# Kernel tuning notes

Measured on AMD Instinct MI355X. Metric: run time of the kernel, lower is better.

The kernel has to match this reference:

```python
import jax, jax.numpy as jnp
import numpy as np

HDIM = 64

def setup_inputs() -> dict:
    key = jax.random.key(0)
    ks = jax.random.split(key, 5)
    B, T, D = 4, 2048, 1024
    x = jax.random.normal(ks[0], (B, T, D), dtype=jnp.float32)
    s = 1.0 / np.sqrt(D)
    W_qkv = jax.random.normal(ks[1], (D, 3 * D), dtype=jnp.float32) * s
    b_qkv = jax.random.normal(ks[2], (3 * D,), dtype=jnp.float32) * 0.02
    W_out = jax.random.normal(ks[3], (D, D), dtype=jnp.float32) * s
    b_out = jax.random.normal(ks[4], (D,), dtype=jnp.float32) * 0.02
    return {"x": x, "W_qkv": W_qkv, "b_qkv": b_qkv, "W_out": W_out, "b_out": b_out}

def reference(x, W_qkv, b_qkv, W_out, b_out):
    B, T, D = x.shape
    H = D // HDIM
    qkv = x @ W_qkv + b_qkv                          # [B,T,3D]
    q, k, v = jnp.split(qkv, 3, axis=-1)
    # [B,T,D] -> [B,H,T,Hdim]
    q = q.reshape(B, T, H, HDIM).transpose(0, 2, 1, 3)
    k = k.reshape(B, T, H, HDIM).transpose(0, 2, 1, 3)
    v = v.reshape(B, T, H, HDIM).transpose(0, 2, 1, 3)
    scores = jnp.einsum('bhqd,bhkd->bhqk', q, k) / jnp.sqrt(jnp.float32(HDIM))
    causal = jnp.tril(jnp.ones((T, T), dtype=bool))
    scores = jnp.where(causal[None, None], scores, -jnp.inf)
    weights = jax.nn.softmax(scores, axis=-1)        # dropout_prob=0 -> identity
    out = jnp.einsum('bhqk,bhkd->bhqd', weights, v)  # [B,H,T,Hdim]
    out = out.transpose(0, 2, 1, 3).reshape(B, T, D)
    return out @ W_out + b_out
```

## Files before the change

### kernel.cpp

```cpp
#include <hip/hip_runtime.h>

typedef __attribute__((ext_vector_type(8))) short short8;
typedef __attribute__((ext_vector_type(4))) short s16x4;
typedef __attribute__((ext_vector_type(4))) float f32x4;

#define AS1 __attribute__((address_space(1)))
#define AS3 __attribute__((address_space(3)))

__device__ __forceinline__ void gload_lds16(const void* g, void* l) {
  __builtin_amdgcn_global_load_lds((const AS1 void*)g, (AS3 void*)l, 16, 0, 0);
}

__device__ __forceinline__ unsigned short f2bf(float f) {
  unsigned int u = __float_as_uint(f);
  u += 0x7fffu + ((u >> 16) & 1u);
  return (unsigned short)(u >> 16);
}

__global__ __launch_bounds__(256) void k_convert(const float* __restrict__ in,
                                                 unsigned short* __restrict__ out) {
  long i = (long)blockIdx.x * 256 + threadIdx.x;
  const float4* p = (const float4*)in + i * 2;
  float4 a = p[0], b = p[1];
  short8 o;
  o[0] = (short)f2bf(a.x); o[1] = (short)f2bf(a.y);
  o[2] = (short)f2bf(a.z); o[3] = (short)f2bf(a.w);
  o[4] = (short)f2bf(b.x); o[5] = (short)f2bf(b.y);
  o[6] = (short)f2bf(b.z); o[7] = (short)f2bf(b.w);
  ((short8*)out)[i] = o;
}

__global__ __launch_bounds__(256) void k_transpose_w(const float* __restrict__ w,
                                                     unsigned short* __restrict__ wt,
                                                     int K, int N) {
  __shared__ float t[64][65];
  const int tilesN = N >> 6;
  const int tk = blockIdx.x / tilesN, tn = blockIdx.x % tilesN;
  const int c = threadIdx.x & 63, r0 = (threadIdx.x >> 6) * 16;
#pragma unroll
  for (int i = 0; i < 16; ++i)
    t[r0 + i][c] = w[(long)(tk * 64 + r0 + i) * N + tn * 64 + c];
  __syncthreads();
#pragma unroll
  for (int i = 0; i < 16; ++i)
    wt[(long)(tn * 64 + r0 + i) * K + tk * 64 + c] = f2bf(t[c][r0 + i]);
}

__global__ __launch_bounds__(256) void k_transpose_v(const unsigned short* __restrict__ qkv,
                                                     unsigned short* __restrict__ vt) {
  __shared__ __align__(16) unsigned short t[64][72];
  const int tt = blockIdx.x & 31, bh = blockIdx.x >> 5;
  const int b = bh >> 4, h = bh & 15;
  const int r = threadIdx.x >> 2, c0 = (threadIdx.x & 3) * 16;
  const unsigned short* src = qkv + (long)(b * 2048 + tt * 64 + r) * 3072 + 2048 + h * 64 + c0;
  *(short8*)&t[r][c0] = *(const short8*)src;
  *(short8*)&t[r][c0 + 8] = *(const short8*)(src + 8);
  __syncthreads();
  short8 w0, w1;
#pragma unroll
  for (int i = 0; i < 8; ++i) w0[i] = (short)t[c0 + i][r];
#pragma unroll
  for (int i = 0; i < 8; ++i) w1[i] = (short)t[c0 + 8 + i][r];
  unsigned short* dst = vt + (long)(bh * 64 + r) * 2048 + tt * 64 + c0;
  *(short8*)dst = w0;
  *(short8*)(dst + 8) = w1;
}

template <int OUT_BF16>
__global__ __launch_bounds__(256) void k_gemm(const unsigned short* __restrict__ A,
                                              const unsigned short* __restrict__ BT,
                                              const float* __restrict__ bias,
                                              void* __restrict__ out,
                                              int M, int N, int K) {
  __shared__ __align__(16) unsigned short As[128 * 64];
  __shared__ __align__(16) unsigned short Bs[128 * 64];
  const int tid = threadIdx.x, lane = tid & 63, wid = tid >> 6;
  const int r16 = lane & 15, khi = lane >> 4;
  const int wr = wid >> 1, wc = wid & 1;
  const int tilesN = N >> 7;
  const int tm = blockIdx.x / tilesN, tn = blockIdx.x % tilesN;
  const long m0 = (long)tm * 128, n0 = (long)tn * 128;
  f32x4 acc[4][4] = {};
  const int srow = tid >> 3, scol = (tid & 7) * 8;

  for (int k0 = 0; k0 < K; k0 += 64) {
#pragma unroll
    for (int call = 0; call < 4; ++call) {
      int row = call * 32 + srow;
      gload_lds16(A + (m0 + row) * K + k0 + scol, &As[call * 2048 + wid * 512]);
      gload_lds16(BT + (n0 + row) * K + k0 + scol, &Bs[call * 2048 + wid * 512]);
    }
    __syncthreads();
#pragma unroll
    for (int kk = 0; kk < 2; ++kk) {
      short8 af[4], bf[4];
#pragma unroll
      for (int m = 0; m < 4; ++m)
        af[m] = *(const short8*)&As[(wr * 64 + m * 16 + r16) * 64 + kk * 32 + khi * 8];
#pragma unroll
      for (int n = 0; n < 4; ++n)
        bf[n] = *(const short8*)&Bs[(wc * 64 + n * 16 + r16) * 64 + kk * 32 + khi * 8];
#pragma unroll
      for (int m = 0; m < 4; ++m)
#pragma unroll
        for (int n = 0; n < 4; ++n)
          acc[m][n] = __builtin_amdgcn_mfma_f32_16x16x32_bf16(af[m], bf[n], acc[m][n], 0, 0, 0);
    }
    __syncthreads();
  }
#pragma unroll
  for (int m = 0; m < 4; ++m) {
    long row = m0 + wr * 64 + m * 16 + khi * 4;
#pragma unroll
    for (int n = 0; n < 4; ++n) {
      int col = (int)n0 + wc * 64 + n * 16 + r16;
      float bv = bias[col];
#pragma unroll
      for (int j = 0; j < 4; ++j) {
        float v = acc[m][n][j] + bv;
        if (OUT_BF16)
          ((unsigned short*)out)[(row + j) * N + col] = f2bf(v);
        else
          ((float*)out)[(row + j) * N + col] = v;
      }
    }
  }
}

__global__ __launch_bounds__(512) void k_attn(const unsigned short* __restrict__ qkv,
                                              const unsigned short* __restrict__ vt,
                                              unsigned short* __restrict__ aout) {
  __shared__ __align__(16) unsigned short Ks[2][64 * 64];
  __shared__ __align__(16) unsigned short VTs[2][64 * 64];
  __shared__ __align__(16) unsigned short Ps[8][16 * 72];
  const int tid = threadIdx.x, lane = tid & 63, wid = tid >> 6;
  const int r16 = lane & 15, khi = lane >> 4;
  const int qt = 15 - (int)(blockIdx.x >> 6), bh = blockIdx.x & 63;
  const int b = bh >> 4, h = bh & 15;
  const long qrow0 = (long)b * 2048 + qt * 128;

  const int srow = wid * 8 + (lane >> 3);
  const int lck = (lane & 7) ^ (srow & 7);
  const unsigned short* kbase =
      qkv + ((long)b * 2048 + srow) * 3072 + 1024 + h * 64 + lck * 8;
  const unsigned short* vbase = vt + ((long)bh * 64 + srow) * 2048 + lck * 8;

  const long qrow = qrow0 + wid * 16 + r16;
  const short8 qf0 = *(const short8*)&qkv[qrow * 3072 + h * 64 + khi * 8];
  const short8 qf1 = *(const short8*)&qkv[qrow * 3072 + h * 64 + 32 + khi * 8];

  gload_lds16(kbase, &Ks[0][wid * 512]);
  gload_lds16(vbase, &VTs[0][wid * 512]);

  const int ktmax = 2 * qt + 1;
  const int ktw = (qt * 128 + wid * 16 + 15) >> 6;
  const int qg = qt * 128 + wid * 16 + r16;
  float m_run = -1e30f, l_run = 0.f;
  f32x4 o[4] = {};

  for (int kt = 0; kt <= ktmax; ++kt) {
    const int cur = kt & 1;
    __builtin_amdgcn_s_barrier();
    if (kt < ktmax) {
      gload_lds16(kbase + (long)(kt + 1) * 64 * 3072, &Ks[cur ^ 1][wid * 512]);
      gload_lds16(vbase + (kt + 1) * 64, &VTs[cur ^ 1][wid * 512]);
      asm volatile("s_waitcnt vmcnt(2)" ::: "memory");
    } else {
      asm volatile("s_waitcnt vmcnt(0)" ::: "memory");
    }
    __builtin_amdgcn_s_barrier();
    if (kt > ktw) continue;

    f32x4 s[4] = {};
    __builtin_amdgcn_s_setprio(1);
#pragma unroll
    for (int kk = 0; kk < 2; ++kk) {
      const int pc = ((kk * 4 + khi) ^ (r16 & 7)) * 8;
      const short8 qf = kk ? qf1 : qf0;
#pragma unroll
      for (int n = 0; n < 4; ++n) {
        short8 kf = *(const short8*)&Ks[cur][(n * 16 + r16) * 64 + pc];
        s[n] = __builtin_amdgcn_mfma_f32_16x16x32_bf16(kf, qf, s[n], 0, 0, 0);
      }
    }
    __builtin_amdgcn_s_setprio(0);

    const bool need_mask = (kt * 64 + 63) > (qt * 128 + wid * 16);
    const int ktB = kt * 64;
#pragma unroll
    for (int n = 0; n < 4; ++n)
#pragma unroll
      for (int j = 0; j < 4; ++j) {
        float v = s[n][j] * 0.125f;
        if (need_mask && (ktB + n * 16 + khi * 4 + j) > qg) v = -1e30f;
        s[n][j] = v;
      }

    float pm = s[0][0];
#pragma unroll
    for (int n = 0; n < 4; ++n)
#pragma unroll
      for (int j = 0; j < 4; ++j) pm = fmaxf(pm, s[n][j]);
    pm = fmaxf(pm, __shfl_xor(pm, 16, 64));
    pm = fmaxf(pm, __shfl_xor(pm, 32, 64));
    const float mn = fmaxf(m_run, pm);
    const float alpha = __expf(m_run - mn);
    m_run = mn;
    float rs = 0.f;
#pragma unroll
    for (int n = 0; n < 4; ++n)
#pragma unroll
      for (int j = 0; j < 4; ++j) {
        float e = __expf(s[n][j] - mn);
        s[n][j] = e;
        rs += e;
      }
    rs += __shfl_xor(rs, 16, 64);
    rs += __shfl_xor(rs, 32, 64);
    l_run = l_run * alpha + rs;
#pragma unroll
    for (int n = 0; n < 4; ++n)
#pragma unroll
      for (int j = 0; j < 4; ++j) o[n][j] *= alpha;

#pragma unroll
    for (int n = 0; n < 4; ++n) {
      s16x4 pw;
#pragma unroll
      for (int j = 0; j < 4; ++j) pw[j] = (short)f2bf(s[n][j]);
      *(s16x4*)&Ps[wid][r16 * 72 + n * 16 + khi * 4] = pw;
    }

    __builtin_amdgcn_s_setprio(1);
#pragma unroll
    for (int kk = 0; kk < 2; ++kk) {
      const short8 pf = *(const short8*)&Ps[wid][r16 * 72 + kk * 32 + khi * 8];
      const int pc = ((kk * 4 + khi) ^ (r16 & 7)) * 8;
#pragma unroll
      for (int n = 0; n < 4; ++n) {
        short8 vf = *(const short8*)&VTs[cur][(n * 16 + r16) * 64 + pc];
        o[n] = __builtin_amdgcn_mfma_f32_16x16x32_bf16(vf, pf, o[n], 0, 0, 0);
      }
    }
    __builtin_amdgcn_s_setprio(0);
  }

  const float inv = 1.f / l_run;
#pragma unroll
  for (int n = 0; n < 4; ++n) {
    s16x4 ow;
#pragma unroll
    for (int j = 0; j < 4; ++j) ow[j] = (short)f2bf(o[n][j] * inv);
    *(s16x4*)&aout[qrow * 1024 + h * 64 + n * 16 + khi * 4] = ow;
  }
}

extern "C" void kernel_launch(void* const* d_in, const int* in_sizes, int n_in,
                              void* d_out, int out_size, void* d_ws, size_t ws_size,
                              hipStream_t stream) {
  (void)in_sizes; (void)n_in; (void)out_size; (void)ws_size;
  const float* x = (const float*)d_in[0];
  const float* Wqkv = (const float*)d_in[1];
  const float* bqkv = (const float*)d_in[2];
  const float* Wout = (const float*)d_in[3];
  const float* bout = (const float*)d_in[4];
  char* ws = (char*)d_ws;
  unsigned short* xb    = (unsigned short*)(ws + 0);
  unsigned short* wqkvt = (unsigned short*)(ws + (16l << 20));
  unsigned short* woutt = (unsigned short*)(ws + (22l << 20));
  unsigned short* qkv   = (unsigned short*)(ws + (24l << 20));
  unsigned short* vt    = (unsigned short*)(ws + (72l << 20));
  unsigned short* aout  = xb;

  k_convert<<<4096, 256, 0, stream>>>(x, xb);
  k_transpose_w<<<768, 256, 0, stream>>>(Wqkv, wqkvt, 1024, 3072);
  k_transpose_w<<<256, 256, 0, stream>>>(Wout, woutt, 1024, 1024);
  k_gemm<1><<<64 * 24, 256, 0, stream>>>(xb, wqkvt, bqkv, qkv, 8192, 3072, 1024);
  k_transpose_v<<<2048, 256, 0, stream>>>(qkv, vt);
  k_attn<<<16 * 64, 512, 0, stream>>>(qkv, vt, aout);
  k_gemm<0><<<64 * 8, 256, 0, stream>>>(aout, woutt, bout, d_out, 8192, 1024, 1024);
}
```

Before: 286.1 us.

## Double-buffer GEMM LDS tiles with XOR swizzle and XCD-aware block remap

The shared GEMM kernel now keeps two LDS buffers per operand, so the next K-tile's global-to-LDS loads are issued before the MFMAs on the current tile, with explicit vmcnt waits and raw barriers. This aims to hide global load latency behind compute. LDS columns are XOR-swizzled by row to cut bank conflicts on the fragment reads, and block IDs are remapped so consecutive tiles share an XCD for L2 reuse. Wave priority is raised during the MFMA section. The costs are double the LDS use, which may lower occupancy, and manual waitcnt logic that relies on exact load counts; the remap also assumes the grid size is a multiple of 8.

```diff
diff --git a/kernel.cpp b/kernel.cpp
--- a/kernel.cpp
+++ b/kernel.cpp
@@ -72,41 +72,65 @@
                                               const float* __restrict__ bias,
                                               void* __restrict__ out,
                                               int M, int N, int K) {
-  __shared__ __align__(16) unsigned short As[128 * 64];
-  __shared__ __align__(16) unsigned short Bs[128 * 64];
+  __shared__ __align__(16) unsigned short As[2][128 * 64];
+  __shared__ __align__(16) unsigned short Bs[2][128 * 64];
   const int tid = threadIdx.x, lane = tid & 63, wid = tid >> 6;
   const int r16 = lane & 15, khi = lane >> 4;
   const int wr = wid >> 1, wc = wid & 1;
   const int tilesN = N >> 7;
-  const int tm = blockIdx.x / tilesN, tn = blockIdx.x % tilesN;
+  const int cpx = gridDim.x >> 3;
+  const int bid = ((int)blockIdx.x & 7) * cpx + ((int)blockIdx.x >> 3);
+  const int tm = bid / tilesN, tn = bid % tilesN;
   const long m0 = (long)tm * 128, n0 = (long)tn * 128;
   f32x4 acc[4][4] = {};
-  const int srow = tid >> 3, scol = (tid & 7) * 8;
-
-  for (int k0 = 0; k0 < K; k0 += 64) {
-#pragma unroll
-    for (int call = 0; call < 4; ++call) {
-      int row = call * 32 + srow;
-      gload_lds16(A + (m0 + row) * K + k0 + scol, &As[call * 2048 + wid * 512]);
-      gload_lds16(BT + (n0 + row) * K + k0 + scol, &Bs[call * 2048 + wid * 512]);
-    }
-    __syncthreads();
+  const int srow = tid >> 3;
+  const int scol = ((tid & 7) ^ (srow & 7)) * 8;
+  const unsigned short* aSrc = A + (m0 + srow) * K + scol;
+  const unsigned short* bSrc = BT + (n0 + srow) * K + scol;
+  unsigned short* aDst = &As[0][0] + tid * 8;
+  unsigned short* bDst = &Bs[0][0] + tid * 8;
+  const int nk = K >> 6;
+
+#pragma unroll
+  for (int call = 0; call < 4; ++call) {
+    gload_lds16(aSrc + (long)call * 32 * K, aDst + call * 2048);
+    gload_lds16(bSrc + (long)call * 32 * K, bDst + call * 2048);
+  }
+
+  int cur = 0;
+  for (int ki = 0; ki < nk; ++ki) {
+    __builtin_amdgcn_s_barrier();
+    if (ki + 1 < nk) {
+      const long k0 = (long)(ki + 1) * 64;
+#pragma unroll
+      for (int call = 0; call < 4; ++call) {
+        gload_lds16(aSrc + (long)call * 32 * K + k0, aDst + (cur ^ 1) * 8192 + call * 2048);
+        gload_lds16(bSrc + (long)call * 32 * K + k0, bDst + (cur ^ 1) * 8192 + call * 2048);
+      }
+      asm volatile("s_waitcnt vmcnt(8)" ::: "memory");
+    } else {
+      asm volatile("s_waitcnt vmcnt(0)" ::: "memory");
+    }
+    __builtin_amdgcn_s_barrier();
+    __builtin_amdgcn_s_setprio(1);
 #pragma unroll
     for (int kk = 0; kk < 2; ++kk) {
+      const int pc = ((kk * 4 + khi) ^ (r16 & 7)) * 8;
       short8 af[4], bf[4];
 #pragma unroll
       for (int m = 0; m < 4; ++m)
-        af[m] = *(const short8*)&As[(wr * 64 + m * 16 + r16) * 64 + kk * 32 + khi * 8];
+        af[m] = *(const short8*)&As[cur][(wr * 64 + m * 16 + r16) * 64 + pc];
 #pragma unroll
       for (int n = 0; n < 4; ++n)
-        bf[n] = *(const short8*)&Bs[(wc * 64 + n * 16 + r16) * 64 + kk * 32 + khi * 8];
+        bf[n] = *(const short8*)&Bs[cur][(wc * 64 + n * 16 + r16) * 64 + pc];
 #pragma unroll
       for (int m = 0; m < 4; ++m)
 #pragma unroll
         for (int n = 0; n < 4; ++n)
           acc[m][n] = __builtin_amdgcn_mfma_f32_16x16x32_bf16(af[m], bf[n], acc[m][n], 0, 0, 0);
     }
-    __syncthreads();
+    __builtin_amdgcn_s_setprio(0);
+    cur ^= 1;
   }
 #pragma unroll
   for (int m = 0; m < 4; ++m) {
```

Measured after the change: 263.2 us. -8.0%, faster.
